# Performance work log

Hardware: AMD Instinct MI355X
Metric: run time of the kernel (lower is better)

The kernel has to match this reference:

```python
import jax, jax.numpy as jnp
import numpy as np

DIM = 128
H = 8
HD = DIM // H
NL = 6
DFF = 2048
EPS = 1e-5
S2S_STEPS = 6


def _ln(x, g, b):
    m = jnp.mean(x, -1, keepdims=True)
    v = jnp.mean(jnp.square(x - m), -1, keepdims=True)
    return (x - m) / jnp.sqrt(v + EPS) * g + b


def _lstm_step(x, h, c, wih, whh, bih, bhh):
    # torch LSTM gate order: i, f, g, o
    gates = x @ wih.T + bih + h @ whh.T + bhh
    i, f, g, o = jnp.split(gates, 4, axis=-1)
    c = jax.nn.sigmoid(f) * c + jax.nn.sigmoid(i) * jnp.tanh(g)
    h = jax.nn.sigmoid(o) * jnp.tanh(c)
    return h, c


def setup_inputs() -> dict:
    key = jax.random.key(0)
    ks = iter(jax.random.split(key, 16))
    n = lambda shape: jax.random.normal(next(ks), shape, jnp.float32) * 0.02
    inp = {
        "data": jax.random.normal(next(ks), (64, 256, 3), jnp.float32),
        "lin0_w": n((DIM, 3)), "lin0_b": jnp.zeros((DIM,), jnp.float32),
        "attn_in_w": n((NL, 3 * DIM, DIM)), "attn_in_b": jnp.zeros((NL, 3 * DIM), jnp.float32),
        "attn_out_w": n((NL, DIM, DIM)), "attn_out_b": jnp.zeros((NL, DIM), jnp.float32),
        "ln1_g": jnp.ones((NL, DIM), jnp.float32), "ln1_b": jnp.zeros((NL, DIM), jnp.float32),
        "ff_w1": n((NL, DFF, DIM)), "ff_b1": jnp.zeros((NL, DFF), jnp.float32),
        "ff_w2": n((NL, DIM, DFF)), "ff_b2": jnp.zeros((NL, DIM), jnp.float32),
        "ln2_g": jnp.ones((NL, DIM), jnp.float32), "ln2_b": jnp.zeros((NL, DIM), jnp.float32),
        "s2s_wih": n((4 * DIM, 2 * DIM)), "s2s_whh": n((4 * DIM, DIM)),
        "s2s_bih": jnp.zeros((4 * DIM,), jnp.float32), "s2s_bhh": jnp.zeros((4 * DIM,), jnp.float32),
        "mem_wih": n((4 * DIM, 2 * DIM)), "mem_whh": n((4 * DIM, DIM)),
        "mem_bih": jnp.zeros((4 * DIM,), jnp.float32), "mem_bhh": jnp.zeros((4 * DIM,), jnp.float32),
        "lin1_w": n((DIM, DIM)), "lin1_b": jnp.zeros((DIM,), jnp.float32),
        "lin3_w": n((1, DIM)), "lin3_b": jnp.zeros((1,), jnp.float32),
    }
    return inp


def reference(data, lin0_w, lin0_b, attn_in_w, attn_in_b, attn_out_w, attn_out_b,
              ln1_g, ln1_b, ff_w1, ff_b1, ff_w2, ff_b2, ln2_g, ln2_b,
              s2s_wih, s2s_whh, s2s_bih, s2s_bhh,
              mem_wih, mem_whh, mem_bih, mem_bhh,
              lin1_w, lin1_b, lin3_w, lin3_b):
    x = jax.nn.relu(data @ lin0_w.T + lin0_b)  # [S=64, B=256, D]
    S, B, _ = x.shape
    # torch TransformerEncoder with batch_first=False: attention over axis 0,
    # axis 1 is the transformer batch. Post-norm layers (norm_first=False), relu FFN.
    for l in range(NL):
        qkv = x @ attn_in_w[l].T + attn_in_b[l]
        q, k, v = jnp.split(qkv, 3, axis=-1)
        q = q.reshape(S, B, H, HD)
        k = k.reshape(S, B, H, HD)
        v = v.reshape(S, B, H, HD)
        scores = jnp.einsum('sbhd,tbhd->bhst', q, k) / np.float32(np.sqrt(HD))
        attn = jax.nn.softmax(scores, axis=-1)
        ao = jnp.einsum('bhst,tbhd->sbhd', attn, v).reshape(S, B, DIM)
        x = _ln(x + ao @ attn_out_w[l].T + attn_out_b[l], ln1_g[l], ln1_b[l])
        ff = jax.nn.relu(x @ ff_w1[l].T + ff_b1[l]) @ ff_w2[l].T + ff_b2[l]
        x = _ln(x + ff, ln2_g[l], ln2_b[l])
    # Set2Set pooling: bidxs assign segment = axis-0 index for each block of
    # num_atoms consecutive rows of flatten(out,0,1), i.e. pool over axis 1.
    q_star = jnp.zeros((S, 2 * DIM), x.dtype)
    h = jnp.zeros((S, DIM), x.dtype)
    c = jnp.zeros((S, DIM), x.dtype)
    for _ in range(S2S_STEPS):
        h, c = _lstm_step(q_star, h, c, s2s_wih, s2s_whh, s2s_bih, s2s_bhh)
        e = jnp.einsum('bnd,bd->bn', x, h)          # [S, num_atoms]
        a = jax.nn.softmax(e, axis=-1)              # segment softmax (uniform segs)
        r = jnp.einsum('bn,bnd->bd', a, x)          # segment weighted sum
        q_star = jnp.concatenate([h, r], axis=-1)   # [S, 2D]
    # memory LSTM: seq_len 1, zero initial state (states=None branch)
    hx = jnp.zeros((S, DIM), x.dtype)
    cx = jnp.zeros((S, DIM), x.dtype)
    hx, cx = _lstm_step(q_star, hx, cx, mem_wih, mem_whh, mem_bih, mem_bhh)
    o = jax.nn.relu(hx @ lin1_w.T + lin1_b)
    v_out = (o @ lin3_w.T + lin3_b)[None]  # [1, S, 1]
    return v_out, hx[None], cx[None]
```

## Files before the change

### kernel.cpp

```cpp
#include <hip/hip_runtime.h>
#include <math.h>


typedef _Float16 __attribute__((ext_vector_type(8))) f16x8;
typedef __attribute__((ext_vector_type(4))) float f32x4;
typedef _Float16 __attribute__((ext_vector_type(2))) h16x2;

__device__ __forceinline__ unsigned short f2h(float f) {
  union { _Float16 h; unsigned short s; } x; x.h = (_Float16)f; return x.s;
}
__device__ __forceinline__ float h2f(unsigned short u) {
  union { unsigned short s; _Float16 h; } x; x.s = u; return (float)x.h;
}
__device__ __forceinline__ unsigned packh(float a, float b) {
  return (unsigned)f2h(a) | ((unsigned)f2h(b) << 16);
}
__device__ __forceinline__ float hlo(unsigned u) {
  union { unsigned short s; _Float16 h; } x; x.s = (unsigned short)(u & 0xffff);
  return (float)x.h;
}
__device__ __forceinline__ float hhi(unsigned u) {
  union { unsigned short s; _Float16 h; } x; x.s = (unsigned short)(u >> 16);
  return (float)x.h;
}
__device__ __forceinline__ float fdot2u(unsigned a, unsigned b, float c) {
#if __has_builtin(__builtin_amdgcn_fdot2)
  union U { unsigned u; h16x2 h; };
  U x, y; x.u = a; y.u = b;
  return __builtin_amdgcn_fdot2(x.h, y.h, c, false);
#else
  return c + hlo(a) * hlo(b) + hhi(a) * hhi(b);
#endif
}
__device__ __forceinline__ float sigf(float x) { return 1.f / (1.f + expf(-x)); }

__device__ __forceinline__ void gl2lds16(const void* g, void* l) {
  __builtin_amdgcn_global_load_lds(
      (const __attribute__((address_space(1))) unsigned int*)g,
      (__attribute__((address_space(3))) unsigned int*)l, 16, 0, 0);
}

__global__ __launch_bounds__(256) void convw_kernel(
    const float* __restrict__ aiw, const float* __restrict__ aow,
    const float* __restrict__ w1, const float* __restrict__ w2,
    const float* __restrict__ wih, const float* __restrict__ whh,
    const float* __restrict__ mwih,
    unsigned short* __restrict__ o0, unsigned short* __restrict__ o1,
    unsigned short* __restrict__ o2, unsigned short* __restrict__ o3,
    unsigned short* __restrict__ o4, unsigned short* __restrict__ o5,
    unsigned short* __restrict__ o6) {
  int i = blockIdx.x * 256 + threadIdx.x;
  if (i < 294912) {
    int l = i / 49152, o = i % 49152;
    int j = o & 7, fr = (o >> 3) & 15, fq = (o >> 7) & 3, ks = (o >> 9) & 3,
        rb = o >> 11;
    o0[i] = f2h(aiw[l * 49152 + (rb * 16 + fr) * 128 + ks * 32 + fq * 8 + j]);
  } else if (i < 393216) {
    int ii = i - 294912;
    int l = ii / 16384, o = ii % 16384;
    int j = o & 7, fr = (o >> 3) & 15, fq = (o >> 7) & 3, ks = (o >> 9) & 3,
        rb = o >> 11;
    o1[ii] = f2h(aow[l * 16384 + (rb * 16 + fr) * 128 + ks * 32 + fq * 8 + j]);
  } else if (i < 1966080) {
    int ii = i - 393216;
    int l = ii >> 18, o = ii & 262143;
    int j = o & 7, fr = (o >> 3) & 15, fq = (o >> 7) & 3, ks = (o >> 9) & 3,
        rb = o >> 11;
    o2[ii] = f2h(w1[l * 262144 + (rb * 16 + fr) * 128 + ks * 32 + fq * 8 + j]);
  } else if (i < 3538944) {
    int ii = i - 1966080;
    int l = ii >> 18, o = ii & 262143;
    int j = o & 7, fr = (o >> 3) & 15, fq = (o >> 7) & 3, ks = (o >> 9) & 63,
        rb = o >> 15;
    o3[ii] = f2h(w2[l * 262144 + (rb * 16 + fr) * 2048 + ks * 32 + fq * 8 + j]);
  } else if (i < 3670016) {
    int j = i - 3538944; o4[j] = f2h(wih[j]);
  } else if (i < 3735552) {
    int j = i - 3670016; o5[j] = f2h(whh[j]);
  } else {
    int j = i - 3735552; o6[j] = f2h(mwih[j]);
  }
}

__global__ __launch_bounds__(256) void lin0_kernel(
    const float* __restrict__ data, const float* __restrict__ w,
    const float* __restrict__ b, float* __restrict__ x,
    unsigned short* __restrict__ xb) {
  int i = blockIdx.x * 256 + threadIdx.x;
  int n = i >> 7, d = i & 127;
  float v = b[d] + data[n * 3 + 0] * w[d * 3 + 0]
                 + data[n * 3 + 1] * w[d * 3 + 1]
                 + data[n * 3 + 2] * w[d * 3 + 2];
  v = fmaxf(v, 0.0f);
  x[i] = v;
  xb[i] = f2h(v);
}

__global__ __launch_bounds__(256, 2) void layer_kernel(
    const unsigned short* __restrict__ xbg,
    const unsigned short* __restrict__ wqkv, const float* __restrict__ bqkv,
    const unsigned short* __restrict__ wout, const float* __restrict__ bout,
    const float* __restrict__ ln1g, const float* __restrict__ ln1b,
    const unsigned short* __restrict__ w1, const float* __restrict__ b1,
    const unsigned short* __restrict__ w2, const float* __restrict__ b2,
    const float* __restrict__ ln2g, const float* __restrict__ ln2b,
    float* __restrict__ xio, unsigned short* __restrict__ xbo) {
  __shared__ __align__(16) unsigned short SM[28672];
  __shared__ float psum[4][32], psq[4][32];
  __shared__ float2 stats[32];
  __shared__ __align__(16) uint4 zchunk;

  unsigned short* Xs = SM;
  unsigned short* Ks = SM + 8192;
  unsigned short* VT = SM + 16384;
  unsigned short* AOs = SM + 16384;
  unsigned short* Qs = SM + 24576;
  unsigned short* Xn = SM + 24576;

  int tid = threadIdx.x, w = tid >> 6, lane = tid & 63;
  int b = blockIdx.x >> 1, half = blockIdx.x & 1;
  int r4 = lane >> 4, cs = lane & 15;
  int fr = lane & 15, fq = lane >> 4;

  if (tid == 0) zchunk = make_uint4(0u, 0u, 0u, 0u);

#pragma unroll
  for (int i = 0; i < 4; i++) {
    int issue = w * 4 + i;
    int row = issue * 4 + r4;
    int g = cs ^ (row & 7);
    gl2lds16(xbg + (size_t)(row * 256 + b) * 128 + g * 8,
             (char*)Xs + issue * 1024);
  }
  __syncthreads();

  {
    f32x4 acc[2][2];
#pragma unroll
    for (int i = 0; i < 2; i++)
#pragma unroll
      for (int j = 0; j < 2; j++) acc[i][j] = (f32x4){0.f, 0.f, 0.f, 0.f};
#pragma unroll
    for (int ks = 0; ks < 4; ks++) {
      f16x8 bf[2];
#pragma unroll
      for (int ni = 0; ni < 2; ni++)
        bf[ni] = *(const f16x8*)(wqkv + (size_t)(w * 2 + ni) * 2048 +
                                 ks * 512 + fq * 128 + fr * 8);
      f16x8 af[2];
#pragma unroll
      for (int mi2 = 0; mi2 < 2; mi2++) {
        int row = half * 32 + mi2 * 16 + fr;
        int kq = (ks * 4 + fq) ^ (row & 7);
        af[mi2] = *(const f16x8*)(Xs + row * 128 + kq * 8);
      }
#pragma unroll
      for (int mi2 = 0; mi2 < 2; mi2++)
#pragma unroll
        for (int ni = 0; ni < 2; ni++)
          acc[mi2][ni] = __builtin_amdgcn_mfma_f32_16x16x32_f16(
              af[mi2], bf[ni], acc[mi2][ni], 0, 0, 0);
    }
#pragma unroll
    for (int ni = 0; ni < 2; ni++) {
      int c = (w * 2 + ni) * 16 + fr;
      float bv = bqkv[c];
#pragma unroll
      for (int mi2 = 0; mi2 < 2; mi2++)
#pragma unroll
        for (int r = 0; r < 4; r++) {
          int prow = mi2 * 16 + fq * 4 + r;
          Qs[prow * 128 + (((c >> 3) ^ (prow & 7)) << 3) + (c & 7)] =
              f2h(acc[mi2][ni][r] + bv);
        }
    }
  }
  {
    f32x4 acc[4][2];
#pragma unroll
    for (int i = 0; i < 4; i++)
#pragma unroll
      for (int j = 0; j < 2; j++) acc[i][j] = (f32x4){0.f, 0.f, 0.f, 0.f};
#pragma unroll
    for (int ks = 0; ks < 4; ks++) {
      f16x8 bf[2];
#pragma unroll
      for (int ni = 0; ni < 2; ni++)
        bf[ni] = *(const f16x8*)(wqkv + (size_t)(8 + w * 2 + ni) * 2048 +
                                 ks * 512 + fq * 128 + fr * 8);
      f16x8 af[4];
#pragma unroll
      for (int mi = 0; mi < 4; mi++) {
        int row = mi * 16 + fr;
        int kq = (ks * 4 + fq) ^ (row & 7);
        af[mi] = *(const f16x8*)(Xs + row * 128 + kq * 8);
      }
#pragma unroll
      for (int mi = 0; mi < 4; mi++)
#pragma unroll
        for (int ni = 0; ni < 2; ni++)
          acc[mi][ni] = __builtin_amdgcn_mfma_f32_16x16x32_f16(
              af[mi], bf[ni], acc[mi][ni], 0, 0, 0);
    }
#pragma unroll
    for (int ni = 0; ni < 2; ni++) {
      int cc = (w * 2 + ni) * 16 + fr;
      float bv = bqkv[128 + cc];
#pragma unroll
      for (int mi = 0; mi < 4; mi++)
#pragma unroll
        for (int r = 0; r < 4; r++) {
          int row = mi * 16 + fq * 4 + r;
          Ks[row * 128 + (((cc >> 3) ^ (row & 7)) << 3) + (cc & 7)] =
              f2h(acc[mi][ni][r] + bv);
        }
    }
  }
  {
    f32x4 acc[4][2];
#pragma unroll
    for (int i = 0; i < 4; i++)
#pragma unroll
      for (int j = 0; j < 2; j++) acc[i][j] = (f32x4){0.f, 0.f, 0.f, 0.f};
#pragma unroll
    for (int ks = 0; ks < 4; ks++) {
      f16x8 bf[2];
#pragma unroll
      for (int ni = 0; ni < 2; ni++)
        bf[ni] = *(const f16x8*)(wqkv + (size_t)(16 + w * 2 + ni) * 2048 +
                                 ks * 512 + fq * 128 + fr * 8);
      f16x8 af[4];
#pragma unroll
      for (int mi = 0; mi < 4; mi++) {
        int row = mi * 16 + fr;
        int kq = (ks * 4 + fq) ^ (row & 7);
        af[mi] = *(const f16x8*)(Xs + row * 128 + kq * 8);
      }
#pragma unroll
      for (int mi = 0; mi < 4; mi++)
#pragma unroll
        for (int ni = 0; ni < 2; ni++)
          acc[mi][ni] = __builtin_amdgcn_mfma_f32_16x16x32_f16(
              af[mi], bf[ni], acc[mi][ni], 0, 0, 0);
    }
#pragma unroll
    for (int ni = 0; ni < 2; ni++) {
      int f = (w * 2 + ni) * 16 + fr;
      float bv = bqkv[256 + f];
#pragma unroll
      for (int mi = 0; mi < 4; mi++)
#pragma unroll
        for (int r = 0; r < 4; r++) {
          int srow = mi * 16 + fq * 4 + r;
          VT[f * 64 + (((srow >> 3) ^ (f & 7)) << 3) + (srow & 7)] =
              f2h(acc[mi][ni][r] + bv);
        }
    }
  }
  __syncthreads();

  f32x4 po[2][2];
#pragma unroll
  for (int i = 0; i < 2; i++)
#pragma unroll
    for (int j = 0; j < 2; j++) po[i][j] = (f32x4){0.f, 0.f, 0.f, 0.f};
  {
    unsigned short* Pb = Xs + w * 2048;
#pragma unroll
    for (int hi = 0; hi < 2; hi++) {
      int h = w * 2 + hi;
      f16x8 afH[2], bfH[4];
#pragma unroll
      for (int mi2 = 0; mi2 < 2; mi2++) {
        int qrow = mi2 * 16 + fr;
        const unsigned short* pa =
            (fq < 2) ? (Qs + qrow * 128 + (((h * 2 + fq) ^ (qrow & 7)) << 3))
                     : (const unsigned short*)&zchunk;
        afH[mi2] = *(const f16x8*)pa;
      }
#pragma unroll
      for (int ti = 0; ti < 4; ti++) {
        int trow = ti * 16 + fr;
        const unsigned short* pb =
            (fq < 2) ? (Ks + trow * 128 + (((h * 2 + fq) ^ (trow & 7)) << 3))
                     : (const unsigned short*)&zchunk;
        bfH[ti] = *(const f16x8*)pb;
      }
      f32x4 sc[2][4];
#pragma unroll
      for (int i = 0; i < 2; i++)
#pragma unroll
        for (int j = 0; j < 4; j++) sc[i][j] = (f32x4){0.f, 0.f, 0.f, 0.f};
#pragma unroll
      for (int mi2 = 0; mi2 < 2; mi2++)
#pragma unroll
        for (int ti = 0; ti < 4; ti++)
          sc[mi2][ti] = __builtin_amdgcn_mfma_f32_16x16x32_f16(
              afH[mi2], bfH[ti], sc[mi2][ti], 0, 0, 0);
#pragma unroll
      for (int mi2 = 0; mi2 < 2; mi2++) {
#pragma unroll
        for (int r = 0; r < 4; r++) {
          float m = -1e30f;
#pragma unroll
          for (int ti = 0; ti < 4; ti++) m = fmaxf(m, sc[mi2][ti][r]);
          m = fmaxf(m, __shfl_xor(m, 1, 64));
          m = fmaxf(m, __shfl_xor(m, 2, 64));
          m = fmaxf(m, __shfl_xor(m, 4, 64));
          m = fmaxf(m, __shfl_xor(m, 8, 64));
          m *= 0.25f;
          float ss = 0.f;
#pragma unroll
          for (int ti = 0; ti < 4; ti++) {
            float p = expf(sc[mi2][ti][r] * 0.25f - m);
            sc[mi2][ti][r] = p;
            ss += p;
          }
          ss += __shfl_xor(ss, 1, 64);
          ss += __shfl_xor(ss, 2, 64);
          ss += __shfl_xor(ss, 4, 64);
          ss += __shfl_xor(ss, 8, 64);
          float inv = 1.f / ss;
          int prow = mi2 * 16 + fq * 4 + r;
#pragma unroll
          for (int ti = 0; ti < 4; ti++) {
            int t = ti * 16 + fr;
            Pb[prow * 64 + (((t >> 3) ^ (prow & 7)) << 3) + (t & 7)] =
                f2h(sc[mi2][ti][r] * inv);
          }
        }
      }
#pragma unroll
      for (int ks2 = 0; ks2 < 2; ks2++) {
        f16x8 af[2], bf;
#pragma unroll
        for (int si2 = 0; si2 < 2; si2++) {
          int prow = si2 * 16 + fr;
          int kq = (ks2 * 4 + fq) ^ (prow & 7);
          af[si2] = *(const f16x8*)(Pb + prow * 64 + kq * 8);
        }
        {
          int vrow = h * 16 + fr;
          int kq = (ks2 * 4 + fq) ^ (vrow & 7);
          bf = *(const f16x8*)(VT + vrow * 64 + kq * 8);
        }
#pragma unroll
        for (int si2 = 0; si2 < 2; si2++)
          po[hi][si2] = __builtin_amdgcn_mfma_f32_16x16x32_f16(
              af[si2], bf, po[hi][si2], 0, 0, 0);
      }
    }
  }
  __syncthreads();
#pragma unroll
  for (int hi = 0; hi < 2; hi++) {
    int c = (w * 2 + hi) * 16 + fr;
#pragma unroll
    for (int si2 = 0; si2 < 2; si2++)
#pragma unroll
      for (int r = 0; r < 4; r++) {
        int arow = si2 * 16 + fq * 4 + r;
        AOs[arow * 128 + (((c >> 3) ^ (arow & 7)) << 3) + (c & 7)] =
            f2h(po[hi][si2][r]);
      }
  }
  __syncthreads();

  {
    f32x4 acc[2][2];
#pragma unroll
    for (int i = 0; i < 2; i++)
#pragma unroll
      for (int j = 0; j < 2; j++) acc[i][j] = (f32x4){0.f, 0.f, 0.f, 0.f};
#pragma unroll
    for (int ks = 0; ks < 4; ks++) {
      f16x8 af[2], bwo[2];
#pragma unroll
      for (int si2 = 0; si2 < 2; si2++) {
        int rowl = si2 * 16 + fr;
        int kq = (ks * 4 + fq) ^ (rowl & 7);
        af[si2] = *(const f16x8*)(AOs + rowl * 128 + kq * 8);
      }
#pragma unroll
      for (int ni = 0; ni < 2; ni++)
        bwo[ni] = *(const f16x8*)(wout + (size_t)(w * 2 + ni) * 2048 +
                                  ks * 512 + fq * 128 + fr * 8);
#pragma unroll
      for (int si2 = 0; si2 < 2; si2++)
#pragma unroll
        for (int ni = 0; ni < 2; ni++)
          acc[si2][ni] = __builtin_amdgcn_mfma_f32_16x16x32_f16(
              af[si2], bwo[ni], acc[si2][ni], 0, 0, 0);
    }
    float vv4[2][2][4];
    float sums[2][4], sqs[2][4];
#pragma unroll
    for (int si2 = 0; si2 < 2; si2++)
#pragma unroll
      for (int r = 0; r < 4; r++) { sums[si2][r] = 0.f; sqs[si2][r] = 0.f; }
#pragma unroll
    for (int ni = 0; ni < 2; ni++) {
      int c = (w * 2 + ni) * 16 + fr;
      float bv = bout[c];
#pragma unroll
      for (int si2 = 0; si2 < 2; si2++)
#pragma unroll
        for (int r = 0; r < 4; r++) {
          int rowl = si2 * 16 + fq * 4 + r;
          int rowg = half * 32 + rowl;
          float v = acc[si2][ni][r] + bv +
                    xio[(size_t)(rowg * 256 + b) * 128 + c];
          vv4[ni][si2][r] = v;
          sums[si2][r] += v;
          sqs[si2][r] += v * v;
        }
    }
#pragma unroll
    for (int d = 1; d < 16; d <<= 1) {
#pragma unroll
      for (int si2 = 0; si2 < 2; si2++)
#pragma unroll
        for (int r = 0; r < 4; r++) {
          sums[si2][r] += __shfl_xor(sums[si2][r], d, 64);
          sqs[si2][r] += __shfl_xor(sqs[si2][r], d, 64);
        }
    }
    if (fr == 0) {
#pragma unroll
      for (int si2 = 0; si2 < 2; si2++)
#pragma unroll
        for (int r = 0; r < 4; r++) {
          int rowl = si2 * 16 + fq * 4 + r;
          psum[w][rowl] = sums[si2][r];
          psq[w][rowl] = sqs[si2][r];
        }
    }
    __syncthreads();
    if (tid < 32) {
      float S = 0.f, Q = 0.f;
#pragma unroll
      for (int ww = 0; ww < 4; ww++) { S += psum[ww][tid]; Q += psq[ww][tid]; }
      float m = S * (1.f / 128.f);
      float var = Q * (1.f / 128.f) - m * m;
      stats[tid] = make_float2(m, rsqrtf(var + 1e-5f));
    }
    __syncthreads();
#pragma unroll
    for (int ni = 0; ni < 2; ni++) {
      int c = (w * 2 + ni) * 16 + fr;
      float gl = ln1g[c], bl = ln1b[c];
#pragma unroll
      for (int si2 = 0; si2 < 2; si2++)
#pragma unroll
        for (int r = 0; r < 4; r++) {
          int rowl = si2 * 16 + fq * 4 + r;
          float2 st2 = stats[rowl];
          float y = (vv4[ni][si2][r] - st2.x) * st2.y * gl + bl;
          Xn[rowl * 128 + (((c >> 3) ^ (rowl & 7)) << 3) + (c & 7)] = f2h(y);
        }
    }
  }
  __syncthreads();

  f16x8 xfragF[4][2];
#pragma unroll
  for (int ks = 0; ks < 4; ks++)
#pragma unroll
    for (int mi2 = 0; mi2 < 2; mi2++) {
      int rowl = mi2 * 16 + fr;
      int kq = (ks * 4 + fq) ^ (rowl & 7);
      xfragF[ks][mi2] = *(const f16x8*)(Xn + rowl * 128 + kq * 8);
    }

  f32x4 acc2[2][2];
#pragma unroll
  for (int i = 0; i < 2; i++)
#pragma unroll
    for (int j = 0; j < 2; j++) acc2[i][j] = (f32x4){0.f, 0.f, 0.f, 0.f};

  for (int c = 0; c < 8; c++) {
    unsigned short* Hcur = SM + (c & 1) * 8192;
    f32x4 acc1[2][4];
#pragma unroll
    for (int i = 0; i < 2; i++)
#pragma unroll
      for (int j = 0; j < 4; j++) acc1[i][j] = (f32x4){0.f, 0.f, 0.f, 0.f};
#pragma unroll
    for (int ks = 0; ks < 4; ks++) {
      f16x8 b1f[4];
#pragma unroll
      for (int ni = 0; ni < 4; ni++)
        b1f[ni] = *(const f16x8*)(w1 + (size_t)(c * 16 + w * 4 + ni) * 2048 +
                                  ks * 512 + fq * 128 + fr * 8);
#pragma unroll
      for (int mi2 = 0; mi2 < 2; mi2++)
#pragma unroll
        for (int ni = 0; ni < 4; ni++)
          acc1[mi2][ni] = __builtin_amdgcn_mfma_f32_16x16x32_f16(
              xfragF[ks][mi2], b1f[ni], acc1[mi2][ni], 0, 0, 0);
    }
#pragma unroll
    for (int ni = 0; ni < 4; ni++) {
      int col = (w * 4 + ni) * 16 + fr;
      float bv = b1[c * 256 + col];
#pragma unroll
      for (int mi2 = 0; mi2 < 2; mi2++)
#pragma unroll
        for (int r = 0; r < 4; r++) {
          int rowl = mi2 * 16 + fq * 4 + r;
          Hcur[rowl * 256 + (((col >> 3) ^ (rowl & 7)) << 3) + (col & 7)] =
              f2h(fmaxf(acc1[mi2][ni][r] + bv, 0.f));
        }
    }
    __syncthreads();
#pragma unroll
    for (int ks2 = 0; ks2 < 8; ks2++) {
      f16x8 af[2], b2f[2];
#pragma unroll
      for (int si2 = 0; si2 < 2; si2++) {
        int rowl = si2 * 16 + fr;
        int kq = (ks2 * 4 + fq) ^ (rowl & 7);
        af[si2] = *(const f16x8*)(Hcur + rowl * 256 + kq * 8);
      }
#pragma unroll
      for (int ni = 0; ni < 2; ni++)
        b2f[ni] = *(const f16x8*)(w2 + (size_t)(w * 2 + ni) * 32768 +
                                  (c * 8 + ks2) * 512 + fq * 128 + fr * 8);
#pragma unroll
      for (int si2 = 0; si2 < 2; si2++)
#pragma unroll
        for (int ni = 0; ni < 2; ni++)
          acc2[si2][ni] = __builtin_amdgcn_mfma_f32_16x16x32_f16(
              af[si2], b2f[ni], acc2[si2][ni], 0, 0, 0);
    }
  }

  {
    float vvo[2][2][4];
    float sums[2][4], sqs[2][4];
#pragma unroll
    for (int si2 = 0; si2 < 2; si2++)
#pragma unroll
      for (int r = 0; r < 4; r++) { sums[si2][r] = 0.f; sqs[si2][r] = 0.f; }
#pragma unroll
    for (int ni = 0; ni < 2; ni++) {
      int c = (w * 2 + ni) * 16 + fr;
      float bv = b2[c];
#pragma unroll
      for (int si2 = 0; si2 < 2; si2++)
#pragma unroll
        for (int r = 0; r < 4; r++) {
          int rowl = si2 * 16 + fq * 4 + r;
          float resid =
              h2f(Xn[rowl * 128 + (((c >> 3) ^ (rowl & 7)) << 3) + (c & 7)]);
          float v = acc2[si2][ni][r] + bv + resid;
          vvo[ni][si2][r] = v;
          sums[si2][r] += v;
          sqs[si2][r] += v * v;
        }
    }
#pragma unroll
    for (int d = 1; d < 16; d <<= 1) {
#pragma unroll
      for (int si2 = 0; si2 < 2; si2++)
#pragma unroll
        for (int r = 0; r < 4; r++) {
          sums[si2][r] += __shfl_xor(sums[si2][r], d, 64);
          sqs[si2][r] += __shfl_xor(sqs[si2][r], d, 64);
        }
    }
    if (fr == 0) {
#pragma unroll
      for (int si2 = 0; si2 < 2; si2++)
#pragma unroll
        for (int r = 0; r < 4; r++) {
          int rowl = si2 * 16 + fq * 4 + r;
          psum[w][rowl] = sums[si2][r];
          psq[w][rowl] = sqs[si2][r];
        }
    }
    __syncthreads();
    if (tid < 32) {
      float S = 0.f, Q = 0.f;
#pragma unroll
      for (int ww = 0; ww < 4; ww++) { S += psum[ww][tid]; Q += psq[ww][tid]; }
      float m = S * (1.f / 128.f);
      float var = Q * (1.f / 128.f) - m * m;
      stats[tid] = make_float2(m, rsqrtf(var + 1e-5f));
    }
    __syncthreads();
#pragma unroll
    for (int ni = 0; ni < 2; ni++) {
      int c = (w * 2 + ni) * 16 + fr;
      float gl = ln2g[c], bl = ln2b[c];
#pragma unroll
      for (int si2 = 0; si2 < 2; si2++)
#pragma unroll
        for (int r = 0; r < 4; r++) {
          int rowl = si2 * 16 + fq * 4 + r;
          float2 st = stats[rowl];
          float y = (vvo[ni][si2][r] - st.x) * st.y * gl + bl;
          size_t o = (size_t)((half * 32 + rowl) * 256 + b) * 128 + c;
          xio[o] = y;
          xbo[o] = f2h(y);
        }
    }
  }
}

__global__ __launch_bounds__(512, 1) void s2s_kernel(
    const unsigned short* __restrict__ xb,
    const unsigned short* __restrict__ wihh,
    const unsigned short* __restrict__ whhh,
    const float* __restrict__ bih, const float* __restrict__ bhh,
    const unsigned short* __restrict__ mwihh,
    const float* __restrict__ mbih, const float* __restrict__ mbhh,
    const float* __restrict__ l1w, const float* __restrict__ l1b,
    const float* __restrict__ l3w, const float* __restrict__ l3b,
    float* __restrict__ out) {
  __shared__ __align__(16) unsigned xl[256 * 65];
  __shared__ __align__(16) unsigned qu[128];
  __shared__ __align__(16) float cst[128];
  __shared__ __align__(16) float gates[512];
  __shared__ __align__(16) float red[256];
  __shared__ __align__(16) float aw[256];
  int s = blockIdx.x, t = threadIdx.x, lane = t & 63, w = t >> 6;

  uint4 wreg[32], ureg[16];
  {
    const uint4* wp = (const uint4*)(wihh + (size_t)t * 256);
#pragma unroll
    for (int i = 0; i < 32; i++) wreg[i] = wp[i];
    const uint4* up = (const uint4*)(whhh + (size_t)t * 128);
#pragma unroll
    for (int i = 0; i < 16; i++) ureg[i] = up[i];
  }

  const uint4* xs4 = (const uint4*)(xb + (size_t)s * 32768);
#pragma unroll
  for (int it = 0; it < 8; it++) {
    int f = it * 512 + t;
    uint4 v = xs4[f];
    int n = f >> 4, jc = (f & 15) * 4;
    unsigned* dst = xl + n * 65 + jc;
    dst[0] = v.x; dst[1] = v.y; dst[2] = v.z; dst[3] = v.w;
  }
  if (t < 128) cst[t] = 0.f;
  __syncthreads();

  const uint4* q4 = (const uint4*)qu;
  float bsum = bih[t] + bhh[t];

  for (int step = 0; step < 6; step++) {
    if (step > 0) {
      float a0 = 0.f, a1 = 0.f, a2 = 0.f, a3 = 0.f;
#pragma unroll
      for (int i = 0; i < 16; i++) {
        uint4 qv = q4[i];
        a0 = fdot2u(wreg[i].x, qv.x, a0);
        a1 = fdot2u(wreg[i].y, qv.y, a1);
        a2 = fdot2u(wreg[i].z, qv.z, a2);
        a3 = fdot2u(wreg[i].w, qv.w, a3);
        a0 = fdot2u(ureg[i].x, qv.x, a0);
        a1 = fdot2u(ureg[i].y, qv.y, a1);
        a2 = fdot2u(ureg[i].z, qv.z, a2);
        a3 = fdot2u(ureg[i].w, qv.w, a3);
      }
#pragma unroll
      for (int i = 16; i < 32; i++) {
        uint4 qv = q4[i];
        a0 = fdot2u(wreg[i].x, qv.x, a0);
        a1 = fdot2u(wreg[i].y, qv.y, a1);
        a2 = fdot2u(wreg[i].z, qv.z, a2);
        a3 = fdot2u(wreg[i].w, qv.w, a3);
      }
      gates[t] = bsum + ((a0 + a1) + (a2 + a3));
    } else {
      gates[t] = bsum;
    }
    __syncthreads();
    if (t < 128) {
      float ig = sigf(gates[t]), fg = sigf(gates[128 + t]);
      float gg = tanhf(gates[256 + t]), og = sigf(gates[384 + t]);
      float cn = fg * cst[t] + ig * gg;
      cst[t] = cn;
      float hn = og * tanhf(cn);
      float hp = __shfl_xor(hn, 1, 64);
      if ((t & 1) == 0) qu[t >> 1] = packh(hn, hp);
    }
    __syncthreads();
    if (step > 0) {
      int n = t >> 1, p = t & 1;
      const unsigned* xr = xl + n * 65 + p * 32;
      float e0 = 0.f, e1 = 0.f;
#pragma unroll 8
      for (int i = 0; i < 32; i += 2) {
        e0 = fdot2u(xr[i], qu[p * 32 + i], e0);
        e1 = fdot2u(xr[i + 1], qu[p * 32 + i + 1], e1);
      }
      float e = e0 + e1;
      e += __shfl_xor(e, 1, 64);
      if (p == 0) red[n] = e;
      __syncthreads();
      float v0 = red[lane], v1 = red[64 + lane];
      float v2 = red[128 + lane], v3 = red[192 + lane];
      float m = fmaxf(fmaxf(v0, v1), fmaxf(v2, v3));
#pragma unroll
      for (int d = 1; d < 64; d <<= 1) m = fmaxf(m, __shfl_xor(m, d, 64));
      float p0 = expf(v0 - m), p1 = expf(v1 - m);
      float p2 = expf(v2 - m), p3 = expf(v3 - m);
      float ss = p0 + p1 + p2 + p3;
#pragma unroll
      for (int d = 1; d < 64; d <<= 1) ss += __shfl_xor(ss, d, 64);
      float Sinv = 1.f / ss;
      if (w == 0) {
        aw[lane] = p0 * Sinv; aw[64 + lane] = p1 * Sinv;
        aw[128 + lane] = p2 * Sinv; aw[192 + lane] = p3 * Sinv;
      }
    } else {
      if (t < 256) aw[t] = 1.f / 256.f;
    }
    __syncthreads();
    {
      int d = t & 127, grp = t >> 7;
      const unsigned* xc = xl + grp * 64 * 65 + (d >> 1);
      int hi = d & 1;
      const float* ap = aw + grp * 64;
      float r = 0.f;
#pragma unroll 8
      for (int n2 = 0; n2 < 64; n2++) {
        unsigned u = xc[n2 * 65];
        r += ap[n2] * (hi ? hhi(u) : hlo(u));
      }
      gates[t] = r;
    }
    __syncthreads();
    if (t < 128) {
      float rd = gates[t] + gates[128 + t] + gates[256 + t] + gates[384 + t];
      float rp = __shfl_xor(rd, 1, 64);
      if ((t & 1) == 0) qu[64 + (t >> 1)] = packh(rd, rp);
    }
    __syncthreads();
  }
  {
    float a0 = 0.f, a1 = 0.f, a2 = 0.f, a3 = 0.f;
    const uint4* mp = (const uint4*)(mwihh + (size_t)t * 256);
#pragma unroll 8
    for (int i = 0; i < 32; i++) {
      uint4 wv = mp[i], qv = q4[i];
      a0 = fdot2u(wv.x, qv.x, a0);
      a1 = fdot2u(wv.y, qv.y, a1);
      a2 = fdot2u(wv.z, qv.z, a2);
      a3 = fdot2u(wv.w, qv.w, a3);
    }
    gates[t] = mbih[t] + mbhh[t] + ((a0 + a1) + (a2 + a3));
  }
  __syncthreads();
  if (t < 128) {
    float ig = sigf(gates[t]);
    float gg = tanhf(gates[256 + t]);
    float og = sigf(gates[384 + t]);
    float cx = ig * gg;
    float hx = og * tanhf(cx);
    cst[t] = hx;
    out[64 + s * 128 + t] = hx;
    out[64 + 8192 + s * 128 + t] = cx;
  }
  __syncthreads();
  if (t < 128) {
    float acc = l1b[t];
    const float4* w4 = (const float4*)(l1w + (size_t)t * 128);
    const float4* h4 = (const float4*)cst;
#pragma unroll 8
    for (int k = 0; k < 32; k++) {
      float4 a = w4[k], b = h4[k];
      acc += a.x * b.x + a.y * b.y + a.z * b.z + a.w * b.w;
    }
    red[t] = fmaxf(acc, 0.f) * l3w[t];
  } else if (t < 256) {
    red[t] = 0.f;
  }
  __syncthreads();
  for (int off = 128; off; off >>= 1) {
    if (t < off) red[t] += red[t + off];
    __syncthreads();
  }
  if (t == 0) out[s] = red[0] + l3b[0];
}

extern "C" void kernel_launch(void* const* d_in, const int* in_sizes, int n_in,
                              void* d_out, int out_size, void* d_ws,
                              size_t ws_size, hipStream_t stream) {
  const float* data       = (const float*)d_in[0];
  const float* lin0_w     = (const float*)d_in[1];
  const float* lin0_b     = (const float*)d_in[2];
  const float* attn_in_w  = (const float*)d_in[3];
  const float* attn_in_b  = (const float*)d_in[4];
  const float* attn_out_w = (const float*)d_in[5];
  const float* attn_out_b = (const float*)d_in[6];
  const float* ln1_g      = (const float*)d_in[7];
  const float* ln1_b      = (const float*)d_in[8];
  const float* ff_w1      = (const float*)d_in[9];
  const float* ff_b1      = (const float*)d_in[10];
  const float* ff_w2      = (const float*)d_in[11];
  const float* ff_b2      = (const float*)d_in[12];
  const float* ln2_g      = (const float*)d_in[13];
  const float* ln2_b      = (const float*)d_in[14];
  const float* s2s_wih    = (const float*)d_in[15];
  const float* s2s_whh    = (const float*)d_in[16];
  const float* s2s_bih    = (const float*)d_in[17];
  const float* s2s_bhh    = (const float*)d_in[18];
  const float* mem_wih    = (const float*)d_in[19];
  const float* mem_bih    = (const float*)d_in[21];
  const float* mem_bhh    = (const float*)d_in[22];
  const float* lin1_w     = (const float*)d_in[23];
  const float* lin1_b     = (const float*)d_in[24];
  const float* lin3_w     = (const float*)d_in[25];
  const float* lin3_b     = (const float*)d_in[26];
  float* out = (float*)d_out;

  char* p = (char*)d_ws;
  float* x = (float*)p;                      p += (size_t)16384 * 128 * 4;
  unsigned short* xb = (unsigned short*)p;   p += (size_t)16384 * 128 * 2;
  unsigned short* wqkv = (unsigned short*)p; p += (size_t)294912 * 2;
  unsigned short* wout = (unsigned short*)p; p += (size_t)98304 * 2;
  unsigned short* w1h = (unsigned short*)p;  p += (size_t)1572864 * 2;
  unsigned short* w2h = (unsigned short*)p;  p += (size_t)1572864 * 2;
  unsigned short* wihh = (unsigned short*)p; p += (size_t)131072 * 2;
  unsigned short* whhh = (unsigned short*)p; p += (size_t)65536 * 2;
  unsigned short* mwihh = (unsigned short*)p; p += (size_t)131072 * 2;

  convw_kernel<<<15104, 256, 0, stream>>>(
      attn_in_w, attn_out_w, ff_w1, ff_w2, s2s_wih, s2s_whh, mem_wih,
      wqkv, wout, w1h, w2h, wihh, whhh, mwihh);
  lin0_kernel<<<8192, 256, 0, stream>>>(data, lin0_w, lin0_b, x, xb);

  for (int l = 0; l < 6; l++) {
    layer_kernel<<<512, 256, 0, stream>>>(
        xb, wqkv + (size_t)l * 49152, attn_in_b + l * 384,
        wout + (size_t)l * 16384, attn_out_b + l * 128,
        ln1_g + l * 128, ln1_b + l * 128,
        w1h + (size_t)l * 262144, ff_b1 + l * 2048,
        w2h + (size_t)l * 262144, ff_b2 + l * 128,
        ln2_g + l * 128, ln2_b + l * 128, x, xb);
  }

  s2s_kernel<<<64, 512, 0, stream>>>(
      xb, wihh, whhh, s2s_bih, s2s_bhh,
      mwihh, mem_bih, mem_bhh, lin1_w, lin1_b, lin3_w, lin3_b, out);
}
```

Baseline: 472.1 us.

## Swap MFMA operand order so accumulators hold contiguous features for vector stores

Swaps the A/B operands of most MFMA calls (weights as A, activations as B), so each lane's four accumulator values are four consecutive output features of one row instead of four rows of one feature. Epilogues then write packed 4-wide fp16 (uint2) and float4 stores, load biases, gammas and residuals as float4, and the LayerNorm row reduction needs only two cross-lane shuffles instead of four per statistic. The goal is fewer scalar LDS and global stores and fewer shuffles per block. For the V projection the operands are unchanged and only the VT transposed store is packed along the sequence axis.

```diff
diff --git a/kernel.cpp b/kernel.cpp
--- a/kernel.cpp
+++ b/kernel.cpp
@@ -14,6 +14,9 @@
 }
 __device__ __forceinline__ unsigned packh(float a, float b) {
   return (unsigned)f2h(a) | ((unsigned)f2h(b) << 16);
+}
+__device__ __forceinline__ uint2 pk4(float a, float b, float c, float d) {
+  return make_uint2(packh(a, b), packh(c, d));
 }
 __device__ __forceinline__ float hlo(unsigned u) {
   union { unsigned short s; _Float16 h; } x; x.s = (unsigned short)(u & 0xffff);
@@ -142,37 +145,37 @@
       for (int j = 0; j < 2; j++) acc[i][j] = (f32x4){0.f, 0.f, 0.f, 0.f};
 #pragma unroll
     for (int ks = 0; ks < 4; ks++) {
-      f16x8 bf[2];
+      f16x8 aw[2];
 #pragma unroll
       for (int ni = 0; ni < 2; ni++)
-        bf[ni] = *(const f16x8*)(wqkv + (size_t)(w * 2 + ni) * 2048 +
+        aw[ni] = *(const f16x8*)(wqkv + (size_t)(w * 2 + ni) * 2048 +
                                  ks * 512 + fq * 128 + fr * 8);
-      f16x8 af[2];
+      f16x8 bx[2];
 #pragma unroll
       for (int mi2 = 0; mi2 < 2; mi2++) {
         int row = half * 32 + mi2 * 16 + fr;
         int kq = (ks * 4 + fq) ^ (row & 7);
-        af[mi2] = *(const f16x8*)(Xs + row * 128 + kq * 8);
+        bx[mi2] = *(const f16x8*)(Xs + row * 128 + kq * 8);
       }
 #pragma unroll
       for (int mi2 = 0; mi2 < 2; mi2++)
 #pragma unroll
         for (int ni = 0; ni < 2; ni++)
           acc[mi2][ni] = __builtin_amdgcn_mfma_f32_16x16x32_f16(
-              af[mi2], bf[ni], acc[mi2][ni], 0, 0, 0);
+              aw[ni], bx[mi2], acc[mi2][ni], 0, 0, 0);
     }
 #pragma unroll
     for (int ni = 0; ni < 2; ni++) {
-      int c = (w * 2 + ni) * 16 + fr;
-      float bv = bqkv[c];
-#pragma unroll
-      for (int mi2 = 0; mi2 < 2; mi2++)
-#pragma unroll
-        for (int r = 0; r < 4; r++) {
-          int prow = mi2 * 16 + fq * 4 + r;
-          Qs[prow * 128 + (((c >> 3) ^ (prow & 7)) << 3) + (c & 7)] =
-              f2h(acc[mi2][ni][r] + bv);
-        }
+      int fb = (w * 2 + ni) * 16 + fq * 4;
+      float4 bv = *(const float4*)&bqkv[fb];
+#pragma unroll
+      for (int mi2 = 0; mi2 < 2; mi2++) {
+        int srow = mi2 * 16 + fr;
+        *(uint2*)(Qs + srow * 128 + (((fb >> 3) ^ (srow & 7)) << 3) +
+                  (fb & 7)) =
+            pk4(acc[mi2][ni][0] + bv.x, acc[mi2][ni][1] + bv.y,
+                acc[mi2][ni][2] + bv.z, acc[mi2][ni][3] + bv.w);
+      }
     }
   }
   {
@@ -183,37 +186,37 @@
       for (int j = 0; j < 2; j++) acc[i][j] = (f32x4){0.f, 0.f, 0.f, 0.f};
 #pragma unroll
     for (int ks = 0; ks < 4; ks++) {
-      f16x8 bf[2];
+      f16x8 aw[2];
 #pragma unroll
       for (int ni = 0; ni < 2; ni++)
-        bf[ni] = *(const f16x8*)(wqkv + (size_t)(8 + w * 2 + ni) * 2048 +
+        aw[ni] = *(const f16x8*)(wqkv + (size_t)(8 + w * 2 + ni) * 2048 +
                                  ks * 512 + fq * 128 + fr * 8);
-      f16x8 af[4];
+      f16x8 bx[4];
 #pragma unroll
       for (int mi = 0; mi < 4; mi++) {
         int row = mi * 16 + fr;
         int kq = (ks * 4 + fq) ^ (row & 7);
-        af[mi] = *(const f16x8*)(Xs + row * 128 + kq * 8);
+        bx[mi] = *(const f16x8*)(Xs + row * 128 + kq * 8);
       }
 #pragma unroll
       for (int mi = 0; mi < 4; mi++)
 #pragma unroll
         for (int ni = 0; ni < 2; ni++)
           acc[mi][ni] = __builtin_amdgcn_mfma_f32_16x16x32_f16(
-              af[mi], bf[ni], acc[mi][ni], 0, 0, 0);
+              aw[ni], bx[mi], acc[mi][ni], 0, 0, 0);
     }
 #pragma unroll
     for (int ni = 0; ni < 2; ni++) {
-      int cc = (w * 2 + ni) * 16 + fr;
-      float bv = bqkv[128 + cc];
-#pragma unroll
-      for (int mi = 0; mi < 4; mi++)
-#pragma unroll
-        for (int r = 0; r < 4; r++) {
-          int row = mi * 16 + fq * 4 + r;
-          Ks[row * 128 + (((cc >> 3) ^ (row & 7)) << 3) + (cc & 7)] =
-              f2h(acc[mi][ni][r] + bv);
-        }
+      int fb = (w * 2 + ni) * 16 + fq * 4;
+      float4 bv = *(const float4*)&bqkv[128 + fb];
+#pragma unroll
+      for (int mi = 0; mi < 4; mi++) {
+        int srow = mi * 16 + fr;
+        *(uint2*)(Ks + srow * 128 + (((fb >> 3) ^ (srow & 7)) << 3) +
+                  (fb & 7)) =
+            pk4(acc[mi][ni][0] + bv.x, acc[mi][ni][1] + bv.y,
+                acc[mi][ni][2] + bv.z, acc[mi][ni][3] + bv.w);
+      }
     }
   }
   {
@@ -224,37 +227,37 @@
       for (int j = 0; j < 2; j++) acc[i][j] = (f32x4){0.f, 0.f, 0.f, 0.f};
 #pragma unroll
     for (int ks = 0; ks < 4; ks++) {
-      f16x8 bf[2];
+      f16x8 bw[2];
 #pragma unroll
       for (int ni = 0; ni < 2; ni++)
-        bf[ni] = *(const f16x8*)(wqkv + (size_t)(16 + w * 2 + ni) * 2048 +
+        bw[ni] = *(const f16x8*)(wqkv + (size_t)(16 + w * 2 + ni) * 2048 +
                                  ks * 512 + fq * 128 + fr * 8);
-      f16x8 af[4];
+      f16x8 ax[4];
 #pragma unroll
       for (int mi = 0; mi < 4; mi++) {
         int row = mi * 16 + fr;
         int kq = (ks * 4 + fq) ^ (row & 7);
-        af[mi] = *(const f16x8*)(Xs + row * 128 + kq * 8);
+        ax[mi] = *(const f16x8*)(Xs + row * 128 + kq * 8);
       }
 #pragma unroll
       for (int mi = 0; mi < 4; mi++)
 #pragma unroll
         for (int ni = 0; ni < 2; ni++)
           acc[mi][ni] = __builtin_amdgcn_mfma_f32_16x16x32_f16(
-              af[mi], bf[ni], acc[mi][ni], 0, 0, 0);
+              ax[mi], bw[ni], acc[mi][ni], 0, 0, 0);
     }
 #pragma unroll
     for (int ni = 0; ni < 2; ni++) {
-      int f = (w * 2 + ni) * 16 + fr;
-      float bv = bqkv[256 + f];
-#pragma unroll
-      for (int mi = 0; mi < 4; mi++)
-#pragma unroll
-        for (int r = 0; r < 4; r++) {
-          int srow = mi * 16 + fq * 4 + r;
-          VT[f * 64 + (((srow >> 3) ^ (f & 7)) << 3) + (srow & 7)] =
-              f2h(acc[mi][ni][r] + bv);
-        }
+      int feat = (w * 2 + ni) * 16 + fr;
+      float bv = bqkv[256 + feat];
+#pragma unroll
+      for (int mi = 0; mi < 4; mi++) {
+        int sb = mi * 16 + fq * 4;
+        *(uint2*)(VT + feat * 64 + (((sb >> 3) ^ (feat & 7)) << 3) +
+                  (sb & 7)) =
+            pk4(acc[mi][ni][0] + bv, acc[mi][ni][1] + bv,
+                acc[mi][ni][2] + bv, acc[mi][ni][3] + bv);
+      }
     }
   }
   __syncthreads();
@@ -332,37 +335,36 @@
       }
 #pragma unroll
       for (int ks2 = 0; ks2 < 2; ks2++) {
-        f16x8 af[2], bf;
+        f16x8 bp[2], avt;
 #pragma unroll
         for (int si2 = 0; si2 < 2; si2++) {
           int prow = si2 * 16 + fr;
           int kq = (ks2 * 4 + fq) ^ (prow & 7);
-          af[si2] = *(const f16x8*)(Pb + prow * 64 + kq * 8);
+          bp[si2] = *(const f16x8*)(Pb + prow * 64 + kq * 8);
         }
         {
           int vrow = h * 16 + fr;
           int kq = (ks2 * 4 + fq) ^ (vrow & 7);
-          bf = *(const f16x8*)(VT + vrow * 64 + kq * 8);
+          avt = *(const f16x8*)(VT + vrow * 64 + kq * 8);
         }
 #pragma unroll
         for (int si2 = 0; si2 < 2; si2++)
           po[hi][si2] = __builtin_amdgcn_mfma_f32_16x16x32_f16(
-              af[si2], bf, po[hi][si2], 0, 0, 0);
+              avt, bp[si2], po[hi][si2], 0, 0, 0);
       }
     }
   }
   __syncthreads();
 #pragma unroll
   for (int hi = 0; hi < 2; hi++) {
-    int c = (w * 2 + hi) * 16 + fr;
-#pragma unroll
-    for (int si2 = 0; si2 < 2; si2++)
-#pragma unroll
-      for (int r = 0; r < 4; r++) {
-        int arow = si2 * 16 + fq * 4 + r;
-        AOs[arow * 128 + (((c >> 3) ^ (arow & 7)) << 3) + (c & 7)] =
-            f2h(po[hi][si2][r]);
-      }
+    int fb = (w * 2 + hi) * 16 + fq * 4;
+#pragma unroll
+    for (int si2 = 0; si2 < 2; si2++) {
+      int srow = si2 * 16 + fr;
+      *(uint2*)(AOs + srow * 128 + (((fb >> 3) ^ (srow & 7)) << 3) +
+                (fb & 7)) =
+          pk4(po[hi][si2][0], po[hi][si2][1], po[hi][si2][2], po[hi][si2][3]);
+    }
   }
   __syncthreads();
 
@@ -374,66 +376,57 @@
       for (int j = 0; j < 2; j++) acc[i][j] = (f32x4){0.f, 0.f, 0.f, 0.f};
 #pragma unroll
     for (int ks = 0; ks < 4; ks++) {
-      f16x8 af[2], bwo[2];
-#pragma unroll
-      for (int si2 = 0; si2 < 2; si2++) {
-        int rowl = si2 * 16 + fr;
-        int kq = (ks * 4 + fq) ^ (rowl & 7);
-        af[si2] = *(const f16x8*)(AOs + rowl * 128 + kq * 8);
-      }
+      f16x8 aw[2], bao[2];
 #pragma unroll
       for (int ni = 0; ni < 2; ni++)
-        bwo[ni] = *(const f16x8*)(wout + (size_t)(w * 2 + ni) * 2048 +
-                                  ks * 512 + fq * 128 + fr * 8);
-#pragma unroll
-      for (int si2 = 0; si2 < 2; si2++)
+        aw[ni] = *(const f16x8*)(wout + (size_t)(w * 2 + ni) * 2048 +
+                                 ks * 512 + fq * 128 + fr * 8);
+#pragma unroll
+      for (int mi2 = 0; mi2 < 2; mi2++) {
+        int row = mi2 * 16 + fr;
+        int kq = (ks * 4 + fq) ^ (row & 7);
+        bao[mi2] = *(const f16x8*)(AOs + row * 128 + kq * 8);
+      }
+#pragma unroll
+      for (int mi2 = 0; mi2 < 2; mi2++)
 #pragma unroll
         for (int ni = 0; ni < 2; ni++)
-          acc[si2][ni] = __builtin_amdgcn_mfma_f32_16x16x32_f16(
-              af[si2], bwo[ni], acc[si2][ni], 0, 0, 0);
-    }
-    float vv4[2][2][4];
-    float sums[2][4], sqs[2][4];
-#pragma unroll
-    for (int si2 = 0; si2 < 2; si2++)
-#pragma unroll
-      for (int r = 0; r < 4; r++) { sums[si2][r] = 0.f; sqs[si2][r] = 0.f; }
+          acc[mi2][ni] = __builtin_amdgcn_mfma_f32_16x16x32_f16(
+              aw[ni], bao[mi2], acc[mi2][ni], 0, 0, 0);
+    }
+    float v4[2][2][4];
+    float psA[2] = {0.f, 0.f}, psQ[2] = {0.f, 0.f};
 #pragma unroll
     for (int ni = 0; ni < 2; ni++) {
-      int c = (w * 2 + ni) * 16 + fr;
-      float bv = bout[c];
-#pragma unroll
-      for (int si2 = 0; si2 < 2; si2++)
-#pragma unroll
-        for (int r = 0; r < 4; r++) {
-          int rowl = si2 * 16 + fq * 4 + r;
-          int rowg = half * 32 + rowl;
-          float v = acc[si2][ni][r] + bv +
-                    xio[(size_t)(rowg * 256 + b) * 128 + c];
-          vv4[ni][si2][r] = v;
-          sums[si2][r] += v;
-          sqs[si2][r] += v * v;
-        }
-    }
-#pragma unroll
-    for (int d = 1; d < 16; d <<= 1) {
-#pragma unroll
-      for (int si2 = 0; si2 < 2; si2++)
-#pragma unroll
-        for (int r = 0; r < 4; r++) {
-          sums[si2][r] += __shfl_xor(sums[si2][r], d, 64);
-          sqs[si2][r] += __shfl_xor(sqs[si2][r], d, 64);
-        }
-    }
-    if (fr == 0) {
-#pragma unroll
-      for (int si2 = 0; si2 < 2; si2++)
-#pragma unroll
-        for (int r = 0; r < 4; r++) {
-          int rowl = si2 * 16 + fq * 4 + r;
-          psum[w][rowl] = sums[si2][r];
-          psq[w][rowl] = sqs[si2][r];
-        }
+      int fb = (w * 2 + ni) * 16 + fq * 4;
+      float4 bv = *(const float4*)&bout[fb];
+#pragma unroll
+      for (int mi2 = 0; mi2 < 2; mi2++) {
+        int rowg = half * 32 + mi2 * 16 + fr;
+        float4 rs = *(const float4*)&xio[(size_t)(rowg * 256 + b) * 128 + fb];
+        float t0 = acc[mi2][ni][0] + bv.x + rs.x;
+        float t1 = acc[mi2][ni][1] + bv.y + rs.y;
+        float t2 = acc[mi2][ni][2] + bv.z + rs.z;
+        float t3 = acc[mi2][ni][3] + bv.w + rs.w;
+        v4[ni][mi2][0] = t0; v4[ni][mi2][1] = t1;
+        v4[ni][mi2][2] = t2; v4[ni][mi2][3] = t3;
+        psA[mi2] += (t0 + t1) + (t2 + t3);
+        psQ[mi2] += (t0 * t0 + t1 * t1) + (t2 * t2 + t3 * t3);
+      }
+    }
+#pragma unroll
+    for (int mi2 = 0; mi2 < 2; mi2++) {
+      psA[mi2] += __shfl_xor(psA[mi2], 16, 64);
+      psA[mi2] += __shfl_xor(psA[mi2], 32, 64);
+      psQ[mi2] += __shfl_xor(psQ[mi2], 16, 64);
+      psQ[mi2] += __shfl_xor(psQ[mi2], 32, 64);
+    }
+    if (fq == 0) {
+#pragma unroll
+      for (int mi2 = 0; mi2 < 2; mi2++) {
+        psum[w][mi2 * 16 + fr] = psA[mi2];
+        psq[w][mi2 * 16 + fr] = psQ[mi2];
+      }
     }
     __syncthreads();
     if (tid < 32) {
@@ -447,17 +440,20 @@
     __syncthreads();
 #pragma unroll
     for (int ni = 0; ni < 2; ni++) {
-      int c = (w * 2 + ni) * 16 + fr;
-      float gl = ln1g[c], bl = ln1b[c];
-#pragma unroll
-      for (int si2 = 0; si2 < 2; si2++)
-#pragma unroll
-        for (int r = 0; r < 4; r++) {
-          int rowl = si2 * 16 + fq * 4 + r;
-          float2 st2 = stats[rowl];
-          float y = (vv4[ni][si2][r] - st2.x) * st2.y * gl + bl;
-          Xn[rowl * 128 + (((c >> 3) ^ (rowl & 7)) << 3) + (c & 7)] = f2h(y);
-        }
+      int fb = (w * 2 + ni) * 16 + fq * 4;
+      float4 g4 = *(const float4*)&ln1g[fb];
+      float4 b4 = *(const float4*)&ln1b[fb];
+#pragma unroll
+      for (int mi2 = 0; mi2 < 2; mi2++) {
+        int srow = mi2 * 16 + fr;
+        float2 st = stats[srow];
+        float y0 = (v4[ni][mi2][0] - st.x) * st.y * g4.x + b4.x;
+        float y1 = (v4[ni][mi2][1] - st.x) * st.y * g4.y + b4.y;
+        float y2 = (v4[ni][mi2][2] - st.x) * st.y * g4.z + b4.z;
+        float y3 = (v4[ni][mi2][3] - st.x) * st.y * g4.w + b4.w;
+        *(uint2*)(Xn + srow * 128 + (((fb >> 3) ^ (srow & 7)) << 3) +
+                  (fb & 7)) = pk4(y0, y1, y2, y3);
+      }
     }
   }
   __syncthreads();
@@ -487,97 +483,91 @@
       for (int j = 0; j < 4; j++) acc1[i][j] = (f32x4){0.f, 0.f, 0.f, 0.f};
 #pragma unroll
     for (int ks = 0; ks < 4; ks++) {
-      f16x8 b1f[4];
+      f16x8 aw1[4];
 #pragma unroll
       for (int ni = 0; ni < 4; ni++)
-        b1f[ni] = *(const f16x8*)(w1 + (size_t)(c * 16 + w * 4 + ni) * 2048 +
+        aw1[ni] = *(const f16x8*)(w1 + (size_t)(c * 16 + w * 4 + ni) * 2048 +
                                   ks * 512 + fq * 128 + fr * 8);
 #pragma unroll
       for (int mi2 = 0; mi2 < 2; mi2++)
 #pragma unroll
         for (int ni = 0; ni < 4; ni++)
           acc1[mi2][ni] = __builtin_amdgcn_mfma_f32_16x16x32_f16(
-              xfragF[ks][mi2], b1f[ni], acc1[mi2][ni], 0, 0, 0);
+              aw1[ni], xfragF[ks][mi2], acc1[mi2][ni], 0, 0, 0);
     }
 #pragma unroll
     for (int ni = 0; ni < 4; ni++) {
-      int col = (w * 4 + ni) * 16 + fr;
-      float bv = b1[c * 256 + col];
+      int hb = (w * 4 + ni) * 16 + fq * 4;
+      float4 bv = *(const float4*)&b1[c * 256 + hb];
+#pragma unroll
+      for (int mi2 = 0; mi2 < 2; mi2++) {
+        int srow = mi2 * 16 + fr;
+        *(uint2*)(Hcur + srow * 256 + (((hb >> 3) ^ (srow & 7)) << 3) +
+                  (hb & 7)) =
+            pk4(fmaxf(acc1[mi2][ni][0] + bv.x, 0.f),
+                fmaxf(acc1[mi2][ni][1] + bv.y, 0.f),
+                fmaxf(acc1[mi2][ni][2] + bv.z, 0.f),
+                fmaxf(acc1[mi2][ni][3] + bv.w, 0.f));
+      }
+    }
+    __syncthreads();
+#pragma unroll
+    for (int ks2 = 0; ks2 < 8; ks2++) {
+      f16x8 aw2[2], bh[2];
+#pragma unroll
+      for (int ni = 0; ni < 2; ni++)
+        aw2[ni] = *(const f16x8*)(w2 + (size_t)(w * 2 + ni) * 32768 +
+                                  (c * 8 + ks2) * 512 + fq * 128 + fr * 8);
+#pragma unroll
+      for (int mi2 = 0; mi2 < 2; mi2++) {
+        int row = mi2 * 16 + fr;
+        int kq = (ks2 * 4 + fq) ^ (row & 7);
+        bh[mi2] = *(const f16x8*)(Hcur + row * 256 + kq * 8);
+      }
 #pragma unroll
       for (int mi2 = 0; mi2 < 2; mi2++)
 #pragma unroll
-        for (int r = 0; r < 4; r++) {
-          int rowl = mi2 * 16 + fq * 4 + r;
-          Hcur[rowl * 256 + (((col >> 3) ^ (rowl & 7)) << 3) + (col & 7)] =
-              f2h(fmaxf(acc1[mi2][ni][r] + bv, 0.f));
-        }
-    }
-    __syncthreads();
-#pragma unroll
-    for (int ks2 = 0; ks2 < 8; ks2++) {
-      f16x8 af[2], b2f[2];
-#pragma unroll
-      for (int si2 = 0; si2 < 2; si2++) {
-        int rowl = si2 * 16 + fr;
-        int kq = (ks2 * 4 + fq) ^ (rowl & 7);
-        af[si2] = *(const f16x8*)(Hcur + rowl * 256 + kq * 8);
-      }
-#pragma unroll
-      for (int ni = 0; ni < 2; ni++)
-        b2f[ni] = *(const f16x8*)(w2 + (size_t)(w * 2 + ni) * 32768 +
-                                  (c * 8 + ks2) * 512 + fq * 128 + fr * 8);
-#pragma unroll
-      for (int si2 = 0; si2 < 2; si2++)
-#pragma unroll
         for (int ni = 0; ni < 2; ni++)
-          acc2[si2][ni] = __builtin_amdgcn_mfma_f32_16x16x32_f16(
-              af[si2], b2f[ni], acc2[si2][ni], 0, 0, 0);
+          acc2[mi2][ni] = __builtin_amdgcn_mfma_f32_16x16x32_f16(
+              aw2[ni], bh[mi2], acc2[mi2][ni], 0, 0, 0);
     }
   }
 
   {
-    float vvo[2][2][4];
-    float sums[2][4], sqs[2][4];
-#pragma unroll
-    for (int si2 = 0; si2 < 2; si2++)
-#pragma unroll
-      for (int r = 0; r < 4; r++) { sums[si2][r] = 0.f; sqs[si2][r] = 0.f; }
+    float v4[2][2][4];
+    float psA[2] = {0.f, 0.f}, psQ[2] = {0.f, 0.f};
 #pragma unroll
     for (int ni = 0; ni < 2; ni++) {
-      int c = (w * 2 + ni) * 16 + fr;
-      float bv = b2[c];
-#pragma unroll
-      for (int si2 = 0; si2 < 2; si2++)
-#pragma unroll
-        for (int r = 0; r < 4; r++) {
-          int rowl = si2 * 16 + fq * 4 + r;
-          float resid =
-              h2f(Xn[rowl * 128 + (((c >> 3) ^ (rowl & 7)) << 3) + (c & 7)]);
-          float v = acc2[si2][ni][r] + bv + resid;
-          vvo[ni][si2][r] = v;
-          sums[si2][r] += v;
-          sqs[si2][r] += v * v;
-        }
-    }
-#pragma unroll
-    for (int d = 1; d < 16; d <<= 1) {
-#pragma unroll
-      for (int si2 = 0; si2 < 2; si2++)
-#pragma unroll
-        for (int r = 0; r < 4; r++) {
-          sums[si2][r] += __shfl_xor(sums[si2][r], d, 64);
-          sqs[si2][r] += __shfl_xor(sqs[si2][r], d, 64);
-        }
-    }
-    if (fr == 0) {
-#pragma unroll
-      for (int si2 = 0; si2 < 2; si2++)
-#pragma unroll
-        for (int r = 0; r < 4; r++) {
-          int rowl = si2 * 16 + fq * 4 + r;
-          psum[w][rowl] = sums[si2][r];
-          psq[w][rowl] = sqs[si2][r];
-        }
+      int fb = (w * 2 + ni) * 16 + fq * 4;
+      float4 bv = *(const float4*)&b2[fb];
+#pragma unroll
+      for (int mi2 = 0; mi2 < 2; mi2++) {
+        int srow = mi2 * 16 + fr;
+        uint2 rz = *(const uint2*)(Xn + srow * 128 +
+                                   (((fb >> 3) ^ (srow & 7)) << 3) + (fb & 7));
+        float t0 = acc2[mi2][ni][0] + bv.x + hlo(rz.x);
+        float t1 = acc2[mi2][ni][1] + bv.y + hhi(rz.x);
+        float t2 = acc2[mi2][ni][2] + bv.z + hlo(rz.y);
+        float t3 = acc2[mi2][ni][3] + bv.w + hhi(rz.y);
+        v4[ni][mi2][0] = t0; v4[ni][mi2][1] = t1;
+        v4[ni][mi2][2] = t2; v4[ni][mi2][3] = t3;
+        psA[mi2] += (t0 + t1) + (t2 + t3);
+        psQ[mi2] += (t0 * t0 + t1 * t1) + (t2 * t2 + t3 * t3);
+      }
+    }
+#pragma unroll
+    for (int mi2 = 0; mi2 < 2; mi2++) {
+      psA[mi2] += __shfl_xor(psA[mi2], 16, 64);
+      psA[mi2] += __shfl_xor(psA[mi2], 32, 64);
+      psQ[mi2] += __shfl_xor(psQ[mi2], 16, 64);
+      psQ[mi2] += __shfl_xor(psQ[mi2], 32, 64);
+    }
+    if (fq == 0) {
+#pragma unroll
+      for (int mi2 = 0; mi2 < 2; mi2++) {
+        psum[w][mi2 * 16 + fr] = psA[mi2];
+        psq[w][mi2 * 16 + fr] = psQ[mi2];
+      }
     }
     __syncthreads();
     if (tid < 32) {
@@ -591,19 +581,21 @@
     __syncthreads();
 #pragma unroll
     for (int ni = 0; ni < 2; ni++) {
-      int c = (w * 2 + ni) * 16 + fr;
-      float gl = ln2g[c], bl = ln2b[c];
-#pragma unroll
-      for (int si2 = 0; si2 < 2; si2++)
-#pragma unroll
-        for (int r = 0; r < 4; r++) {
-          int rowl = si2 * 16 + fq * 4 + r;
-          float2 st = stats[rowl];
-          float y = (vvo[ni][si2][r] - st.x) * st.y * gl + bl;
-          size_t o = (size_t)((half * 32 + rowl) * 256 + b) * 128 + c;
-          xio[o] = y;
-          xbo[o] = f2h(y);
-        }
+      int fb = (w * 2 + ni) * 16 + fq * 4;
+      float4 g4 = *(const float4*)&ln2g[fb];
+      float4 b4 = *(const float4*)&ln2b[fb];
+#pragma unroll
+      for (int mi2 = 0; mi2 < 2; mi2++) {
+        int srow = mi2 * 16 + fr;
+        float2 st = stats[srow];
+        float y0 = (v4[ni][mi2][0] - st.x) * st.y * g4.x + b4.x;
+        float y1 = (v4[ni][mi2][1] - st.x) * st.y * g4.y + b4.y;
+        float y2 = (v4[ni][mi2][2] - st.x) * st.y * g4.z + b4.z;
+        float y3 = (v4[ni][mi2][3] - st.x) * st.y * g4.w + b4.w;
+        size_t o = (size_t)((half * 32 + srow) * 256 + b) * 128 + fb;
+        *(float4*)&xio[o] = make_float4(y0, y1, y2, y3);
+        *(uint2*)&xbo[o] = pk4(y0, y1, y2, y3);
+      }
     }
   }
 }
```

Measured after the change: 467.1 us. About the same (-1.1%).
